# Kernel tuning notes

Hardware: AMD Instinct MI355X
Metric: run time of the kernel (lower is better)

The kernel has to match this reference:

```python
import jax, jax.numpy as jnp
import numpy as np

DIM = 256          # channels
HEADS = 8
KS = 3             # kernel_size
DIL = (1, 2, 3, 4) # dilation rates
ND = len(DIL)
HEAD_DIM = DIM // HEADS
SCALE = HEAD_DIM ** -0.5
DPG = DIM // ND    # channels per dilation group
EPS = 1e-5


def setup_inputs() -> dict:
    key = jax.random.key(0)
    ks = jax.random.split(key, 4)
    B, H, W = 8, 64, 64
    vi = jax.random.normal(ks[0], (B, DIM, H, W), jnp.float32)
    ir = jax.random.normal(ks[1], (B, DIM, H, W), jnp.float32)
    w_qkv = jax.random.normal(ks[2], (3 * DIM, DIM), jnp.float32) * 0.02  # 1x1 conv, no bias (qkv_bias=False)
    proj_w = jax.random.normal(ks[3], (DIM, DIM), jnp.float32) * 0.02     # nn.Linear weight
    proj_b = jnp.zeros((DIM,), jnp.float32)
    ln_g = jnp.ones((DIM,), jnp.float32)
    ln_b = jnp.zeros((DIM,), jnp.float32)
    return dict(vi=vi, ir=ir, w_qkv=w_qkv, proj_w=proj_w, proj_b=proj_b, ln_g=ln_g, ln_b=ln_b)


def _unfold(t, dil):
    # t: [B, d, H, W] -> [B, d, KS*KS, H, W], same layout as nn.Unfold(KS, dil, pad=dil*(KS-1)//2)
    B, d, H, W = t.shape
    pad = dil * (KS - 1) // 2
    tp = jnp.pad(t, ((0, 0), (0, 0), (pad, pad), (pad, pad)))
    patches = [tp[:, :, i * dil:i * dil + H, j * dil:j * dil + W]
               for i in range(KS) for j in range(KS)]
    return jnp.stack(patches, axis=2)


def _dilate_attention(q, k, v, dil):
    # q,k,v: [B, d, H, W] with d = DPG; returns [B, H, W, d]
    B, d, H, W = q.shape
    h = d // HEAD_DIM
    N = H * W
    kk = KS * KS
    qf = q.reshape(B, h, HEAD_DIM, N)                      # b h d n
    kf = _unfold(k, dil).reshape(B, h, HEAD_DIM, kk, N)    # b h d k n
    vf = _unfold(v, dil).reshape(B, h, HEAD_DIM, kk, N)
    attn = jax.nn.softmax(jnp.einsum('bhdn,bhdkn->bhnk', qf, kf) * SCALE, axis=-1)
    out = jnp.einsum('bhnk,bhdkn->bhnd', attn, vf)         # b h n d
    return out.transpose(0, 2, 1, 3).reshape(B, H, W, d)   # channel = head*HEAD_DIM + c


def _dilate_block(x, w_qkv, proj_w, proj_b, ln_g, ln_b):
    # x: [B, C, H, W]; DilateBlock: permute -> LN -> MultiDilatelocalAttention -> residual -> permute back
    B, C, H, W = x.shape
    xn = x.transpose(0, 2, 3, 1)                           # B H W C
    mu = jnp.mean(xn, -1, keepdims=True)
    var = jnp.var(xn, -1, keepdims=True)
    xn = (xn - mu) * jax.lax.rsqrt(var + EPS) * ln_g + ln_b
    xc = xn.transpose(0, 3, 1, 2)                          # B C H W
    # 1x1 conv qkv -> [B, 3, ND, DPG, H, W]
    qkv = jnp.einsum('oc,bchw->bohw', w_qkv, xc).reshape(B, 3, ND, DPG, H, W)
    outs = [_dilate_attention(qkv[:, 0, i], qkv[:, 1, i], qkv[:, 2, i], DIL[i])
            for i in range(ND)]                            # each [B, H, W, DPG]
    y = jnp.stack(outs, axis=3).reshape(B, H, W, C)        # channel = dil_idx*DPG + c
    y = y @ proj_w.T + proj_b                              # nn.Linear
    return x + y.transpose(0, 3, 1, 2)                     # residual, back to B C H W


def reference(vi, ir, w_qkv, proj_w, proj_b, ln_g, ln_b):
    sub = vi - ir
    div = _dilate_block(sub, w_qkv, proj_w, proj_b, ln_g, ln_b)
    o = jnp.matmul(vi, div)   # batched [H,W]@[H,W] over (B, C)
    return (o, o)
```

## Files before the change

### kernel.cpp

```cpp
#include <hip/hip_runtime.h>
#include <math.h>

#define B_ 8
#define C_ 256
#define N_ 4096
#define NPOS 32768
#define SCALE_ 0.1767766952966369f
#define EPS_ 1e-5f

typedef __attribute__((ext_vector_type(8))) short bf16x8;
typedef __attribute__((ext_vector_type(8))) unsigned short u16x8;
typedef __attribute__((ext_vector_type(4))) float f32x4;

__device__ __forceinline__ unsigned short f2bf(float f) {
  union { float f; unsigned u; } v; v.f = f;
  unsigned r = v.u + 0x7fff + ((v.u >> 16) & 1);
  return (unsigned short)(r >> 16);
}
__device__ __forceinline__ float bf2f(unsigned short u) {
  union { unsigned u; float f; } v; v.u = ((unsigned)u) << 16; return v.f;
}
__device__ __forceinline__ float blo(unsigned u) {
  union { unsigned u; float f; } v; v.u = u << 16; return v.f;
}
__device__ __forceinline__ float bhi(unsigned u) {
  union { unsigned u; float f; } v; v.u = u & 0xffff0000u; return v.f;
}

#define GLD_LDS16(g, l) \
  __builtin_amdgcn_global_load_lds((const __attribute__((address_space(1))) unsigned int*)(g), \
                                   (__attribute__((address_space(3))) unsigned int*)(l), 16, 0, 0)

__global__ __launch_bounds__(256) void k_pre(
    const float* __restrict__ vi, const float* __restrict__ ir,
    const float* __restrict__ wq, const float* __restrict__ pw,
    const float* __restrict__ ln_g, const float* __restrict__ ln_b,
    unsigned short* __restrict__ wdst,
    unsigned short* __restrict__ subB, unsigned short* __restrict__ viB,
    unsigned short* __restrict__ xn)
{
  __shared__ float tile[C_ * 33];
  __shared__ float redS[8][32], redS2[8][32];
  __shared__ float meanS[32], rstdS[32];
  int t = threadIdx.x;
  if (blockIdx.x < 256) {
    int i4 = blockIdx.x * 256 + t;
    float4 v = (i4 < 49152) ? ((const float4*)wq)[i4] : ((const float4*)pw)[i4 - 49152];
    ushort4 o;
    o.x = f2bf(v.x); o.y = f2bf(v.y); o.z = f2bf(v.z); o.w = f2bf(v.w);
    ((ushort4*)wdst)[i4] = o;
    return;
  }
  int blk = blockIdx.x - 256;
  int b = blk >> 7;
  int y = (blk >> 1) & 63;
  int half = blk & 1;
  size_t base = (size_t)b * C_ * N_ + (size_t)y * 64 + half * 32;
  #pragma unroll
  for (int it = 0; it < 8; ++it) {
    int c = it * 32 + (t >> 3);
    int xq = (t & 7) * 4;
    size_t g = base + (size_t)c * N_ + xq;
    float4 v4 = *(const float4*)&vi[g];
    float4 i4 = *(const float4*)&ir[g];
    float4 s4;
    s4.x = v4.x - i4.x; s4.y = v4.y - i4.y; s4.z = v4.z - i4.z; s4.w = v4.w - i4.w;
    ushort4 sb, vb;
    sb.x = f2bf(s4.x); sb.y = f2bf(s4.y); sb.z = f2bf(s4.z); sb.w = f2bf(s4.w);
    vb.x = f2bf(v4.x); vb.y = f2bf(v4.y); vb.z = f2bf(v4.z); vb.w = f2bf(v4.w);
    *(ushort4*)&subB[g] = sb;
    *(ushort4*)&viB[g] = vb;
    tile[c * 33 + xq + 0] = s4.x;
    tile[c * 33 + xq + 1] = s4.y;
    tile[c * 33 + xq + 2] = s4.z;
    tile[c * 33 + xq + 3] = s4.w;
  }
  __syncthreads();
  {
    int p = t & 31, grp = t >> 5;
    float s = 0.f, s2 = 0.f;
    #pragma unroll
    for (int cc = 0; cc < 32; ++cc) {
      float v = tile[(grp * 32 + cc) * 33 + p];
      s += v; s2 += v * v;
    }
    redS[grp][p] = s; redS2[grp][p] = s2;
  }
  __syncthreads();
  if (t < 32) {
    float s = 0.f, s2 = 0.f;
    #pragma unroll
    for (int g2 = 0; g2 < 8; ++g2) { s += redS[g2][t]; s2 += redS2[g2][t]; }
    float mu = s * (1.f / 256.f);
    float var = s2 * (1.f / 256.f) - mu * mu;
    meanS[t] = mu;
    rstdS[t] = rsqrtf(var + EPS_);
  }
  __syncthreads();
  int c = t;
  float gg = ln_g[c], bb = ln_b[c];
  size_t xbase = ((size_t)b * N_ + (size_t)y * 64 + half * 32) * C_;
  for (int p = 0; p < 32; ++p) {
    float v = (tile[c * 33 + p] - meanS[p]) * rstdS[p] * gg + bb;
    xn[xbase + (size_t)p * C_ + c] = f2bf(v);
  }
}

template<int EPI, int NT>
__global__ __launch_bounds__(256) void k_gemm_mfma(
    const unsigned short* __restrict__ A,
    const unsigned short* __restrict__ Bw,
    unsigned short* __restrict__ Cout,
    const float* __restrict__ bias,
    const unsigned short* __restrict__ subB,
    int ldc)
{
  __shared__ __align__(16) unsigned short As[128 * 32];
  __shared__ __align__(16) unsigned short Bs[128 * 32];
  __shared__ __align__(16) unsigned short Cs[64 * 136];
  int flat = blockIdx.x;
  int xcd = flat & 7;
  int l = flat >> 3;
  int ml = l / NT;
  int nn = l - ml * NT;
  int m0 = (xcd * 32 + ml) * 128;
  int n0 = nn * 128;
  int tid = threadIdx.x;
  int wv = tid >> 6;
  int lane = tid & 63;
  int mw = (wv >> 1) * 64, nw = (wv & 1) * 64;
  int r = lane & 15, q = lane >> 4;

  int seg0 = wv * 2;
  int srow0 = seg0 * 16 + (lane >> 2);
  int scol = (lane & 3) * 8;
  const unsigned short* ga0 = A  + (size_t)(m0 + srow0) * 256 + scol;
  const unsigned short* ga1 = ga0 + 16 * 256;
  const unsigned short* gb0 = Bw + (size_t)(n0 + srow0) * 256 + scol;
  const unsigned short* gb1 = gb0 + 16 * 256;
  unsigned short* la0 = &As[seg0 * 512];
  unsigned short* la1 = la0 + 512;
  unsigned short* lb0 = &Bs[seg0 * 512];
  unsigned short* lb1 = lb0 + 512;

  f32x4 acc[4][4];
  #pragma unroll
  for (int i = 0; i < 4; ++i)
    #pragma unroll
    for (int j = 0; j < 4; ++j)
      acc[i][j] = (f32x4){0.f, 0.f, 0.f, 0.f};

  for (int k0 = 0; k0 < 256; k0 += 32) {
    GLD_LDS16(ga0 + k0, la0);
    GLD_LDS16(ga1 + k0, la1);
    GLD_LDS16(gb0 + k0, lb0);
    GLD_LDS16(gb1 + k0, lb1);
    __syncthreads();
    bf16x8 af[4], bfr[4];
    #pragma unroll
    for (int mt = 0; mt < 4; ++mt)
      af[mt] = *(const bf16x8*)&As[(mw + mt * 16 + r) * 32 + q * 8];
    #pragma unroll
    for (int nt = 0; nt < 4; ++nt)
      bfr[nt] = *(const bf16x8*)&Bs[(nw + nt * 16 + r) * 32 + q * 8];
    #pragma unroll
    for (int mt = 0; mt < 4; ++mt)
      #pragma unroll
      for (int nt = 0; nt < 4; ++nt)
        acc[mt][nt] = __builtin_amdgcn_mfma_f32_16x16x32_bf16(af[mt], bfr[nt], acc[mt][nt], 0, 0, 0);
    __syncthreads();
  }

  int b = m0 >> 12;
  int nn0 = m0 & 4095;
  #pragma unroll
  for (int pass = 0; pass < 2; ++pass) {
    __syncthreads();
    if (EPI == 0) {
      if ((wv >> 1) == pass) {
        #pragma unroll
        for (int mt = 0; mt < 4; ++mt) {
          int lr = mt * 16 + q * 4;
          #pragma unroll
          for (int nt = 0; nt < 4; ++nt) {
            int col = nw + nt * 16 + r;
            #pragma unroll
            for (int rr = 0; rr < 4; ++rr)
              Cs[(lr + rr) * 136 + col] = f2bf(acc[mt][nt][rr]);
          }
        }
      }
    } else {
      if ((wv & 1) == pass) {
        #pragma unroll
        for (int nt = 0; nt < 4; ++nt) {
          int lr = nt * 16 + r;
          #pragma unroll
          for (int mt = 0; mt < 4; ++mt) {
            int pc = mw + mt * 16 + q * 4;
            #pragma unroll
            for (int rr = 0; rr < 4; ++rr)
              Cs[lr * 136 + pc + rr] = f2bf(acc[mt][nt][rr]);
          }
        }
      }
    }
    __syncthreads();
    if (EPI == 0) {
      #pragma unroll
      for (int cc = 0; cc < 4; ++cc) {
        int ch = cc * 256 + tid;
        int row = ch >> 4, cg = ch & 15;
        u16x8 cv = *(const u16x8*)&Cs[row * 136 + cg * 8];
        int m = m0 + pass * 64 + row;
        *(u16x8*)&Cout[(size_t)m * ldc + n0 + cg * 8] = cv;
      }
    } else {
      #pragma unroll
      for (int cc = 0; cc < 4; ++cc) {
        int ch = cc * 256 + tid;
        int row = ch >> 4, cg = ch & 15;
        u16x8 cv = *(const u16x8*)&Cs[row * 136 + cg * 8];
        int c = n0 + pass * 64 + row;
        size_t idx = ((size_t)(b * 256 + c)) * 4096 + nn0 + cg * 8;
        u16x8 sv = *(const u16x8*)&subB[idx];
        float bb = bias[c];
        u16x8 ov;
        #pragma unroll
        for (int e = 0; e < 8; ++e)
          ov[e] = f2bf(bf2f((unsigned short)cv[e]) + bb + bf2f((unsigned short)sv[e]));
        *(u16x8*)&Cout[idx] = ov;
      }
    }
  }
}

__global__ __launch_bounds__(256) void k_attn(
    const unsigned short* __restrict__ qkv,
    unsigned short* __restrict__ y)
{
  int t = threadIdx.x;
  int sub = t >> 2;
  int lane4 = t & 3;
  int item = blockIdx.x * 64 + sub;
  int ih = item & 7;
  int p = item >> 3;
  int i = ih >> 1, h = ih & 1;
  int dil = i + 1;
  int b = p >> 12;
  int n = p & 4095;
  int py = n >> 6, px = n & 63;
  int off = i * 64 + h * 32 + lane4 * 8;
  const unsigned short* base = qkv + off;

  uint4 qw = *(const uint4*)(base + (size_t)p * 768);
  float q0 = blo(qw.x), q1 = bhi(qw.x), q2 = blo(qw.y), q3 = bhi(qw.y),
        q4 = blo(qw.z), q5 = bhi(qw.z), q6 = blo(qw.w), q7 = bhi(qw.w);

  int pj[9];
  #pragma unroll
  for (int j = 0; j < 9; ++j) {
    int ny = py + (j / 3 - 1) * dil;
    int nx = px + (j % 3 - 1) * dil;
    bool ok = ((unsigned)ny < 64u) && ((unsigned)nx < 64u);
    pj[j] = ok ? ((b << 12) + (ny << 6) + nx) : -1;
  }

  float sc[9];
  #pragma unroll
  for (int j = 0; j < 9; ++j) {
    float s = 0.f;
    if (pj[j] >= 0) {
      uint4 kw = *(const uint4*)(base + 256 + (size_t)pj[j] * 768);
      s  = q0 * blo(kw.x) + q1 * bhi(kw.x);
      s += q2 * blo(kw.y) + q3 * bhi(kw.y);
      s += q4 * blo(kw.z) + q5 * bhi(kw.z);
      s += q6 * blo(kw.w) + q7 * bhi(kw.w);
    }
    s += __shfl_xor(s, 1, 4);
    s += __shfl_xor(s, 2, 4);
    sc[j] = s * SCALE_;
  }

  float mx = sc[0];
  #pragma unroll
  for (int j = 1; j < 9; ++j) mx = fmaxf(mx, sc[j]);
  float e[9], ssum = 0.f;
  #pragma unroll
  for (int j = 0; j < 9; ++j) { e[j] = __expf(sc[j] - mx); ssum += e[j]; }
  float inv = 1.f / ssum;

  float o0 = 0.f, o1 = 0.f, o2 = 0.f, o3 = 0.f, o4 = 0.f, o5 = 0.f, o6 = 0.f, o7 = 0.f;
  #pragma unroll
  for (int j = 0; j < 9; ++j) {
    if (pj[j] >= 0) {
      float w = e[j] * inv;
      uint4 vw = *(const uint4*)(base + 512 + (size_t)pj[j] * 768);
      o0 += w * blo(vw.x); o1 += w * bhi(vw.x);
      o2 += w * blo(vw.y); o3 += w * bhi(vw.y);
      o4 += w * blo(vw.z); o5 += w * bhi(vw.z);
      o6 += w * blo(vw.w); o7 += w * bhi(vw.w);
    }
  }

  u16x8 ov;
  ov[0] = f2bf(o0); ov[1] = f2bf(o1); ov[2] = f2bf(o2); ov[3] = f2bf(o3);
  ov[4] = f2bf(o4); ov[5] = f2bf(o5); ov[6] = f2bf(o6); ov[7] = f2bf(o7);
  *(u16x8*)(y + (size_t)p * 256 + off) = ov;
}

__global__ __launch_bounds__(256) void k_bmm(
    const unsigned short* __restrict__ viB,
    const unsigned short* __restrict__ divmB,
    float* __restrict__ out)
{
  __shared__ __align__(16) unsigned short Vs[64 * 72];
  __shared__ __align__(16) unsigned short Ds[64 * 72];
  int bc = blockIdx.x;
  size_t base = (size_t)bc * 4096;
  int t = threadIdx.x;
  {
    int flat = t * 16;
    int row = flat >> 6, col = flat & 63;
    u16x8 v0 = *(const u16x8*)&viB[base + flat];
    u16x8 v1 = *(const u16x8*)&viB[base + flat + 8];
    *(u16x8*)&Vs[row * 72 + col] = v0;
    *(u16x8*)&Vs[row * 72 + col + 8] = v1;
    u16x8 d0 = *(const u16x8*)&divmB[base + flat];
    u16x8 d1 = *(const u16x8*)&divmB[base + flat + 8];
    #pragma unroll
    for (int e = 0; e < 8; ++e) {
      Ds[(col + e) * 72 + row] = (unsigned short)d0[e];
      Ds[(col + 8 + e) * 72 + row] = (unsigned short)d1[e];
    }
  }
  __syncthreads();
  int w = t >> 6, lane = t & 63;
  int r = lane & 15, q = lane >> 4;
  int wi = (w >> 1) * 32, wj = (w & 1) * 32;
  f32x4 acc[2][2];
  #pragma unroll
  for (int i = 0; i < 2; ++i)
    #pragma unroll
    for (int j = 0; j < 2; ++j)
      acc[i][j] = (f32x4){0.f, 0.f, 0.f, 0.f};
  #pragma unroll
  for (int ks = 0; ks < 2; ++ks) {
    bf16x8 a[2], bfr[2];
    #pragma unroll
    for (int ti = 0; ti < 2; ++ti)
      a[ti] = *(const bf16x8*)&Vs[(wi + ti * 16 + r) * 72 + ks * 32 + q * 8];
    #pragma unroll
    for (int tj = 0; tj < 2; ++tj)
      bfr[tj] = *(const bf16x8*)&Ds[(wj + tj * 16 + r) * 72 + ks * 32 + q * 8];
    #pragma unroll
    for (int ti = 0; ti < 2; ++ti)
      #pragma unroll
      for (int tj = 0; tj < 2; ++tj)
        acc[ti][tj] = __builtin_amdgcn_mfma_f32_16x16x32_bf16(a[ti], bfr[tj], acc[ti][tj], 0, 0, 0);
  }
  #pragma unroll
  for (int ti = 0; ti < 2; ++ti)
    #pragma unroll
    for (int tj = 0; tj < 2; ++tj)
      #pragma unroll
      for (int rr = 0; rr < 4; ++rr) {
        int row = wi + ti * 16 + q * 4 + rr;
        int col = wj + tj * 16 + r;
        float v = acc[ti][tj][rr];
        out[base + row * 64 + col] = v;
        out[8388608ull + base + row * 64 + col] = v;
      }
}

extern "C" void kernel_launch(void* const* d_in, const int* in_sizes, int n_in,
                              void* d_out, int out_size, void* d_ws, size_t ws_size,
                              hipStream_t stream) {
  const float* vi     = (const float*)d_in[0];
  const float* ir     = (const float*)d_in[1];
  const float* w_qkv  = (const float*)d_in[2];
  const float* proj_w = (const float*)d_in[3];
  const float* proj_b = (const float*)d_in[4];
  const float* ln_g   = (const float*)d_in[5];
  const float* ln_b   = (const float*)d_in[6];
  float* out = (float*)d_out;
  char* ws = (char*)d_ws;
  unsigned short* subB = (unsigned short*)(ws);
  unsigned short* qkvb = (unsigned short*)(ws + 16777216);
  unsigned short* divmB= (unsigned short*)(ws + 16777216);
  unsigned short* xnb  = (unsigned short*)(ws + 67108864);
  unsigned short* yb   = (unsigned short*)(ws + 83886080);
  unsigned short* viB  = (unsigned short*)(ws + 100663296);
  unsigned short* wqb  = (unsigned short*)(ws + 117440512);
  unsigned short* pwb  = wqb + 196608;

  k_pre<<<1280, 256, 0, stream>>>(vi, ir, w_qkv, proj_w, ln_g, ln_b, wqb, subB, viB, xnb);
  k_gemm_mfma<0, 6><<<1536, 256, 0, stream>>>(xnb, wqb, qkvb, nullptr, nullptr, 768);
  k_attn<<<4096, 256, 0, stream>>>(qkvb, yb);
  k_gemm_mfma<1, 2><<<512, 256, 0, stream>>>(yb, pwb, divmB, proj_b, subB, 0);
  k_bmm<<<2048, 256, 0, stream>>>(viB, divmB, out);
}
```

Measured before the change: 211.1 us.

## Restructure LayerNorm prep kernel with bf16 swizzled tile and shuffle reductions

The k_pre LayerNorm path now keeps a bf16 transposed tile with an XOR swizzle instead of a padded fp32 tile. Per-position sums are accumulated in registers during the load and reduced with warp shuffles, replacing a separate LDS reduction pass. The output write becomes 16-byte vectorized rows with gamma and beta cached in shared memory, and the launch-bounds occupancy hint is raised. One trade-off is that LayerNorm is now applied to bf16-rounded values rather than fp32, which adds a little rounding error.

New measurement: 220.0 us. 4.2% more time.

```diff
diff --git a/kernel.cpp b/kernel.cpp
--- a/kernel.cpp
+++ b/kernel.cpp
@@ -31,7 +31,7 @@
   __builtin_amdgcn_global_load_lds((const __attribute__((address_space(1))) unsigned int*)(g), \
                                    (__attribute__((address_space(3))) unsigned int*)(l), 16, 0, 0)
 
-__global__ __launch_bounds__(256) void k_pre(
+__global__ __launch_bounds__(256, 8) void k_pre(
     const float* __restrict__ vi, const float* __restrict__ ir,
     const float* __restrict__ wq, const float* __restrict__ pw,
     const float* __restrict__ ln_g, const float* __restrict__ ln_b,
@@ -39,9 +39,10 @@
     unsigned short* __restrict__ subB, unsigned short* __restrict__ viB,
     unsigned short* __restrict__ xn)
 {
-  __shared__ float tile[C_ * 33];
-  __shared__ float redS[8][32], redS2[8][32];
+  __shared__ __align__(16) unsigned short tile[32 * 256];
+  __shared__ float redS[4][32], redS2[4][32];
   __shared__ float meanS[32], rstdS[32];
+  __shared__ float sG[256], sB[256];
   int t = threadIdx.x;
   if (blockIdx.x < 256) {
     int i4 = blockIdx.x * 256 + t;
@@ -56,53 +57,77 @@
   int y = (blk >> 1) & 63;
   int half = blk & 1;
   size_t base = (size_t)b * C_ * N_ + (size_t)y * 64 + half * 32;
+  sG[t] = ln_g[t];
+  sB[t] = ln_b[t];
+  int g = t >> 3;
+  int k8 = t & 7;
+  int xq = k8 * 4;
+  int swz = k8 << 3;
+  float s0 = 0.f, s1 = 0.f, s2 = 0.f, s3 = 0.f;
+  float q0 = 0.f, q1 = 0.f, q2 = 0.f, q3 = 0.f;
   #pragma unroll
   for (int it = 0; it < 8; ++it) {
-    int c = it * 32 + (t >> 3);
-    int xq = (t & 7) * 4;
-    size_t g = base + (size_t)c * N_ + xq;
-    float4 v4 = *(const float4*)&vi[g];
-    float4 i4 = *(const float4*)&ir[g];
-    float4 s4;
-    s4.x = v4.x - i4.x; s4.y = v4.y - i4.y; s4.z = v4.z - i4.z; s4.w = v4.w - i4.w;
+    int c = it * 32 + g;
+    size_t ga = base + (size_t)c * N_ + xq;
+    float4 v4 = *(const float4*)&vi[ga];
+    float4 i4 = *(const float4*)&ir[ga];
+    float4 sv;
+    sv.x = v4.x - i4.x; sv.y = v4.y - i4.y; sv.z = v4.z - i4.z; sv.w = v4.w - i4.w;
     ushort4 sb, vb;
-    sb.x = f2bf(s4.x); sb.y = f2bf(s4.y); sb.z = f2bf(s4.z); sb.w = f2bf(s4.w);
+    sb.x = f2bf(sv.x); sb.y = f2bf(sv.y); sb.z = f2bf(sv.z); sb.w = f2bf(sv.w);
     vb.x = f2bf(v4.x); vb.y = f2bf(v4.y); vb.z = f2bf(v4.z); vb.w = f2bf(v4.w);
-    *(ushort4*)&subB[g] = sb;
-    *(ushort4*)&viB[g] = vb;
-    tile[c * 33 + xq + 0] = s4.x;
-    tile[c * 33 + xq + 1] = s4.y;
-    tile[c * 33 + xq + 2] = s4.z;
-    tile[c * 33 + xq + 3] = s4.w;
-  }
-  __syncthreads();
-  {
-    int p = t & 31, grp = t >> 5;
-    float s = 0.f, s2 = 0.f;
-    #pragma unroll
-    for (int cc = 0; cc < 32; ++cc) {
-      float v = tile[(grp * 32 + cc) * 33 + p];
-      s += v; s2 += v * v;
-    }
-    redS[grp][p] = s; redS2[grp][p] = s2;
+    *(ushort4*)&subB[ga] = sb;
+    *(ushort4*)&viB[ga] = vb;
+    int cs = c ^ swz;
+    tile[(xq + 0) * 256 + cs] = sb.x;
+    tile[(xq + 1) * 256 + cs] = sb.y;
+    tile[(xq + 2) * 256 + cs] = sb.z;
+    tile[(xq + 3) * 256 + cs] = sb.w;
+    s0 += sv.x; q0 += sv.x * sv.x;
+    s1 += sv.y; q1 += sv.y * sv.y;
+    s2 += sv.z; q2 += sv.z * sv.z;
+    s3 += sv.w; q3 += sv.w * sv.w;
+  }
+  #pragma unroll
+  for (int m = 8; m <= 32; m <<= 1) {
+    s0 += __shfl_xor(s0, m); q0 += __shfl_xor(q0, m);
+    s1 += __shfl_xor(s1, m); q1 += __shfl_xor(q1, m);
+    s2 += __shfl_xor(s2, m); q2 += __shfl_xor(q2, m);
+    s3 += __shfl_xor(s3, m); q3 += __shfl_xor(q3, m);
+  }
+  int w = t >> 6, lt = t & 63;
+  if ((lt >> 3) == 0) {
+    redS[w][xq + 0] = s0; redS2[w][xq + 0] = q0;
+    redS[w][xq + 1] = s1; redS2[w][xq + 1] = q1;
+    redS[w][xq + 2] = s2; redS2[w][xq + 2] = q2;
+    redS[w][xq + 3] = s3; redS2[w][xq + 3] = q3;
   }
   __syncthreads();
   if (t < 32) {
-    float s = 0.f, s2 = 0.f;
-    #pragma unroll
-    for (int g2 = 0; g2 < 8; ++g2) { s += redS[g2][t]; s2 += redS2[g2][t]; }
+    float s = redS[0][t] + redS[1][t] + redS[2][t] + redS[3][t];
+    float ss = redS2[0][t] + redS2[1][t] + redS2[2][t] + redS2[3][t];
     float mu = s * (1.f / 256.f);
-    float var = s2 * (1.f / 256.f) - mu * mu;
+    float var = ss * (1.f / 256.f) - mu * mu;
     meanS[t] = mu;
     rstdS[t] = rsqrtf(var + EPS_);
   }
   __syncthreads();
-  int c = t;
-  float gg = ln_g[c], bb = ln_b[c];
-  size_t xbase = ((size_t)b * N_ + (size_t)y * 64 + half * 32) * C_;
-  for (int p = 0; p < 32; ++p) {
-    float v = (tile[c * 33 + p] - meanS[p]) * rstdS[p] * gg + bb;
-    xn[xbase + (size_t)p * C_ + c] = f2bf(v);
+  int pos = t >> 3;
+  float mu = meanS[pos], rs = rstdS[pos];
+  int swzr = (pos >> 2) & 7;
+  size_t xrow = ((size_t)b * N_ + (size_t)y * 64 + half * 32 + pos) * 256;
+  #pragma unroll
+  for (int j = 0; j < 4; ++j) {
+    int ci = (t & 7) + 8 * j;
+    u16x8 tv = *(const u16x8*)&tile[pos * 256 + ((ci ^ swzr) * 8)];
+    int c0 = ci * 8;
+    u16x8 ov;
+    #pragma unroll
+    for (int e = 0; e < 8; ++e) {
+      float v = bf2f((unsigned short)tv[e]);
+      ov[e] = f2bf((v - mu) * rs * sG[c0 + e] + sB[c0 + e]);
+    }
+    *(u16x8*)&xn[xrow + c0] = ov;
   }
 }
 
```
